# Performance work log

Measured on AMD Instinct MI355X. Metric: run time of the kernel, lower is better.

## Reference

```python
import jax, jax.numpy as jnp
import numpy as np

Q_DIM = 512
K_DIM = 512
HID = 512


def setup_inputs() -> dict:
    key = jax.random.key(0)
    k1, k2, k3, k4, k5, k6 = jax.random.split(key, 6)
    b, n_q, s = 4, 64, 1024
    queries = jax.random.normal(k1, (b, n_q, Q_DIM), dtype=jnp.float32)
    keys = jax.random.normal(k2, (b, s, K_DIM), dtype=jnp.float32)
    values = jax.random.normal(k3, (b, s, 512), dtype=jnp.float32)
    lim1 = 1.0 / np.sqrt(Q_DIM + K_DIM)
    W1 = jax.random.uniform(k4, (HID, Q_DIM + K_DIM), minval=-lim1, maxval=lim1, dtype=jnp.float32)
    b1 = jax.random.uniform(k5, (HID,), minval=-lim1, maxval=lim1, dtype=jnp.float32)
    lim2 = 1.0 / np.sqrt(HID)
    w2 = jax.random.uniform(k6, (HID,), minval=-lim2, maxval=lim2, dtype=jnp.float32)
    return {"queries": queries, "keys": keys, "values": values,
            "W1": W1, "b1": b1, "w2": w2}


def reference(queries, keys, values, W1, b1, w2):
    # linear1 on concat([q, k]) == W1q @ q + W1k @ k (split the weight),
    # avoiding materializing the concatenated [b, n_q, s, q_v+k_v] tensor.
    W1q = W1[:, :Q_DIM]  # [hid, q_dim]
    W1k = W1[:, Q_DIM:]  # [hid, k_dim]
    q_proj = jnp.einsum('bqd,hd->bqh', queries, W1q)          # [b, n_q, hid]
    k_proj = jnp.einsum('bsd,hd->bsh', keys, W1k) + b1        # [b, s, hid]
    hidden = jnp.tanh(q_proj[:, :, None, :] + k_proj[:, None, :, :])  # [b, n_q, s, hid]
    scores = jnp.einsum('bqsh,h->bqs', hidden, w2)            # [b, n_q, s]
    attn = jax.nn.softmax(scores, axis=2)                     # softmax over key axis
    final = jnp.einsum('bqs,bsv->bqv', attn, values)          # [b, n_q, v_dim]
    return final
```

## Files before the change

### kernel.cpp

```cpp
#include <hip/hip_runtime.h>


static constexpr int SLEN = 1024;
static constexpr int DIM  = 512;
static constexpr float TANH_SCALE = 2.885390081777927f;

typedef __attribute__((ext_vector_type(8))) short bf16x8;
typedef __attribute__((ext_vector_type(4))) float f32x4;

__device__ __forceinline__ float fast_exp2(float x) { return __builtin_amdgcn_exp2f(x); }
__device__ __forceinline__ float fast_rcp(float x)  { return __builtin_amdgcn_rcpf(x); }

__device__ __forceinline__ unsigned int f2bf(float f) {
    unsigned int u = __float_as_uint(f);
    u += 0x7FFF + ((u >> 16) & 1);
    return u >> 16;
}

__device__ __forceinline__ void async_copy16(const void* g, void* l) {
    __builtin_amdgcn_global_load_lds(
        (const __attribute__((address_space(1))) unsigned int*)g,
        (__attribute__((address_space(3))) unsigned int*)l, 16, 0, 0);
}

__global__ __launch_bounds__(256) void convert_bf16(
    const float* __restrict__ q, const float* __restrict__ k,
    const float* __restrict__ w, unsigned short* __restrict__ qb,
    unsigned short* __restrict__ kb, unsigned short* __restrict__ wb)
{
    int id = blockIdx.x * 256 + threadIdx.x;
    const float* src; unsigned short* dst; int off;
    if (id < 32768)        { src = q; dst = qb; off = id; }
    else if (id < 557056)  { src = k; dst = kb; off = id - 32768; }
    else                   { src = w; dst = wb; off = id - 557056; }
    float4 v = ((const float4*)src)[off];
    ushort4 o;
    o.x = (unsigned short)f2bf(v.x); o.y = (unsigned short)f2bf(v.y);
    o.z = (unsigned short)f2bf(v.z); o.w = (unsigned short)f2bf(v.w);
    ((ushort4*)dst)[off] = o;
}

__global__ __launch_bounds__(256) void proj_mfma(
    const unsigned short* __restrict__ qb, const unsigned short* __restrict__ kb,
    const unsigned short* __restrict__ wb, const float* __restrict__ b1,
    float* __restrict__ qp, float* __restrict__ kp)
{
    __shared__ __align__(16) unsigned short As[64][64];
    __shared__ __align__(16) unsigned short Ws[64][64];

    const int bx = blockIdx.x;
    const unsigned short* A; float* C; const float* bias; int mb, nb, col_off;
    if (bx < 512) {
        A = kb; C = kp; bias = b1; col_off = 512;
        mb = (bx >> 3) * 64; nb = (bx & 7) * 64;
    } else {
        int b2 = bx - 512;
        A = qb; C = qp; bias = nullptr; col_off = 0;
        mb = (b2 >> 3) * 64; nb = (b2 & 7) * 64;
    }

    const int t = threadIdx.x;
    const int l = t & 63;
    const int wv = t >> 6;
    const int wm = (wv & 1) * 32;
    const int wn = (wv >> 1) * 32;
    const int lane16 = l & 15;
    const int quad   = l >> 4;
    const int r8   = l >> 3;
    const int schk = (l & 7) ^ r8;

    f32x4 acc[2][2] = {{{0.f,0.f,0.f,0.f},{0.f,0.f,0.f,0.f}},
                       {{0.f,0.f,0.f,0.f},{0.f,0.f,0.f,0.f}}};

    for (int kc = 0; kc < DIM; kc += 64) {
#pragma unroll
        for (int i = 0; i < 2; ++i) {
            int rbase = wv * 16 + i * 8;
            async_copy16(A + (size_t)(mb + rbase + r8) * DIM + kc + schk * 8, &As[rbase][0]);
            async_copy16(wb + (size_t)(nb + rbase + r8) * 1024 + col_off + kc + schk * 8, &Ws[rbase][0]);
        }
        __syncthreads();

#pragma unroll
        for (int ks = 0; ks < 2; ++ks) {
            int cc = ks * 4 + quad;
            int sw = (cc ^ (lane16 & 7)) << 3;
            bf16x8 a0  = *(const bf16x8*)&As[wm + lane16][sw];
            bf16x8 a1  = *(const bf16x8*)&As[wm + 16 + lane16][sw];
            bf16x8 b0  = *(const bf16x8*)&Ws[wn + lane16][sw];
            bf16x8 b1v = *(const bf16x8*)&Ws[wn + 16 + lane16][sw];
            acc[0][0] = __builtin_amdgcn_mfma_f32_16x16x32_bf16(a0, b0,  acc[0][0], 0, 0, 0);
            acc[0][1] = __builtin_amdgcn_mfma_f32_16x16x32_bf16(a0, b1v, acc[0][1], 0, 0, 0);
            acc[1][0] = __builtin_amdgcn_mfma_f32_16x16x32_bf16(a1, b0,  acc[1][0], 0, 0, 0);
            acc[1][1] = __builtin_amdgcn_mfma_f32_16x16x32_bf16(a1, b1v, acc[1][1], 0, 0, 0);
        }
        __syncthreads();
    }

#pragma unroll
    for (int mi = 0; mi < 2; ++mi) {
#pragma unroll
        for (int ni = 0; ni < 2; ++ni) {
            int col = nb + wn + 16 * ni + lane16;
            float bv = bias ? bias[col] : 0.0f;
#pragma unroll
            for (int r = 0; r < 4; ++r) {
                int row = mb + wm + 16 * mi + quad * 4 + r;
                C[(size_t)row * DIM + col] = (acc[mi][ni][r] + bv) * TANH_SCALE;
            }
        }
    }
}

__global__ __launch_bounds__(256) void scores_kernel(
    const float* __restrict__ qp, const float* __restrict__ kp,
    const float* __restrict__ w2, float* __restrict__ sc)
{
    __shared__ __align__(16) float qs[16][68];
    __shared__ __align__(16) float ks[32][68];
    __shared__ __align__(16) float ws2[256];
    const int t     = threadIdx.x;
    const int sb    = blockIdx.x * 32;
    const int qt    = blockIdx.y & 3;
    const int half  = blockIdx.y >> 2;
    const int kbase = half * 256;
    const int qrow0 = blockIdx.z * 64 + qt * 16;
    const int krow0 = blockIdx.z * 1024 + sb;
    float* sch = sc + (size_t)half * 256 * SLEN;

    if (t < 64) *(float4*)&ws2[t << 2] = *(const float4*)(w2 + kbase + (t << 2));

    const int tq = t >> 4;
    const int ts = t & 15;
    float acc0 = 0.f, acc1 = 0.f;

    for (int kc = 0; kc < 256; kc += 64) {
        {
            int r = t >> 4, g = (t & 15) << 2;
            *(float4*)&qs[r][g] = *(const float4*)(qp + (size_t)(qrow0 + r) * DIM + kbase + kc + g);
        }
#pragma unroll
        for (int rr = 0; rr < 2; ++rr) {
            int idx = t + rr * 256;
            int r = idx >> 4, g = (idx & 15) << 2;
            *(float4*)&ks[r][g] = *(const float4*)(kp + (size_t)(krow0 + r) * DIM + kbase + kc + g);
        }
        __syncthreads();
#pragma unroll
        for (int k4 = 0; k4 < 16; ++k4) {
            float4 qv = *(const float4*)&qs[tq][k4 << 2];
            float4 k0 = *(const float4*)&ks[ts][k4 << 2];
            float4 k1 = *(const float4*)&ks[ts + 16][k4 << 2];
            float4 wv = *(const float4*)&ws2[kc + (k4 << 2)];
            acc0 = fmaf(wv.x, fast_rcp(1.0f + fast_exp2(qv.x + k0.x)), acc0);
            acc1 = fmaf(wv.x, fast_rcp(1.0f + fast_exp2(qv.x + k1.x)), acc1);
            acc0 = fmaf(wv.y, fast_rcp(1.0f + fast_exp2(qv.y + k0.y)), acc0);
            acc1 = fmaf(wv.y, fast_rcp(1.0f + fast_exp2(qv.y + k1.y)), acc1);
            acc0 = fmaf(wv.z, fast_rcp(1.0f + fast_exp2(qv.z + k0.z)), acc0);
            acc1 = fmaf(wv.z, fast_rcp(1.0f + fast_exp2(qv.z + k1.z)), acc1);
            acc0 = fmaf(wv.w, fast_rcp(1.0f + fast_exp2(qv.w + k0.w)), acc0);
            acc1 = fmaf(wv.w, fast_rcp(1.0f + fast_exp2(qv.w + k1.w)), acc1);
        }
        __syncthreads();
    }
    sch[(size_t)(qrow0 + tq) * SLEN + sb + ts]      = acc0;
    sch[(size_t)(qrow0 + tq) * SLEN + sb + ts + 16] = acc1;
}

__global__ __launch_bounds__(256) void softmax_kernel(
    const float* __restrict__ sc, float* __restrict__ attn)
{
    const int row = blockIdx.x;
    const int t   = threadIdx.x;
    __shared__ float redm[4];
    __shared__ float reds[4];
    float4 a = *(const float4*)(sc + (size_t)row * SLEN + (t << 2));
    float4 b = *(const float4*)(sc + (size_t)(256 + row) * SLEN + (t << 2));
    float4 v;
    v.x = a.x + b.x; v.y = a.y + b.y; v.z = a.z + b.z; v.w = a.w + b.w;
    float mn = fminf(fminf(v.x, v.y), fminf(v.z, v.w));
#pragma unroll
    for (int off = 32; off; off >>= 1) mn = fminf(mn, __shfl_xor(mn, off, 64));
    if ((t & 63) == 0) redm[t >> 6] = mn;
    __syncthreads();
    mn = fminf(fminf(redm[0], redm[1]), fminf(redm[2], redm[3]));
    float4 e;
    e.x = fast_exp2((mn - v.x) * TANH_SCALE);
    e.y = fast_exp2((mn - v.y) * TANH_SCALE);
    e.z = fast_exp2((mn - v.z) * TANH_SCALE);
    e.w = fast_exp2((mn - v.w) * TANH_SCALE);
    float s = e.x + e.y + e.z + e.w;
#pragma unroll
    for (int off = 32; off; off >>= 1) s += __shfl_xor(s, off, 64);
    if ((t & 63) == 0) reds[t >> 6] = s;
    __syncthreads();
    s = reds[0] + reds[1] + reds[2] + reds[3];
    float r = fast_rcp(s);
    e.x *= r; e.y *= r; e.z *= r; e.w *= r;
    *(float4*)(attn + (size_t)row * SLEN + (t << 2)) = e;
}

__global__ __launch_bounds__(256) void av_gemm(
    const float* __restrict__ attn, const float* __restrict__ values,
    float* __restrict__ pt)
{
    __shared__ __align__(16) float As[32][68];
    __shared__ __align__(16) float Bs[32][68];
    const int t  = threadIdx.x;
    const int nb = blockIdx.x * 64;
    const int kt = blockIdx.y;
    const int kb = kt * 128;
    const int b  = blockIdx.z;
    const int tx = t & 15, ty = t >> 4;
    float acc[4][4] = {};
    for (int kc = 0; kc < 128; kc += 32) {
        const int k0 = kb + kc;
#pragma unroll
        for (int r = 0; r < 2; ++r) {
            int idx = t + r * 256;
            int m   = idx >> 3;
            int k4  = (idx & 7) << 2;
            float4 av = *(const float4*)(attn + (size_t)(b * 64 + m) * SLEN + k0 + k4);
            As[k4 + 0][m] = av.x; As[k4 + 1][m] = av.y;
            As[k4 + 2][m] = av.z; As[k4 + 3][m] = av.w;
            int kk = idx >> 4;
            int g  = (idx & 15) << 2;
            *(float4*)&Bs[kk][g] =
                *(const float4*)(values + (size_t)(b * 1024 + k0 + kk) * DIM + nb + g);
        }
        __syncthreads();
#pragma unroll
        for (int k = 0; k < 32; ++k) {
            float4 a  = *(const float4*)&As[k][ty << 2];
            float4 bv = *(const float4*)&Bs[k][tx << 2];
            float am[4] = {a.x, a.y, a.z, a.w};
            float bn[4] = {bv.x, bv.y, bv.z, bv.w};
#pragma unroll
            for (int i = 0; i < 4; ++i)
#pragma unroll
                for (int j = 0; j < 4; ++j)
                    acc[i][j] = fmaf(am[i], bn[j], acc[i][j]);
        }
        __syncthreads();
    }
#pragma unroll
    for (int i = 0; i < 4; ++i) {
        int row = b * 64 + (ty << 2) + i;
        float4 o;
        o.x = acc[i][0]; o.y = acc[i][1]; o.z = acc[i][2]; o.w = acc[i][3];
        *(float4*)(pt + ((size_t)kt * 256 + row) * DIM + nb + (tx << 2)) = o;
    }
}

__global__ __launch_bounds__(256) void reduce_kernel(
    const float* __restrict__ pt, float* __restrict__ out)
{
    int idx = blockIdx.x * 256 + threadIdx.x;
    const float4* p = (const float4*)pt;
    float4 a = p[idx];
#pragma unroll
    for (int k = 1; k < 8; ++k) {
        float4 v = p[k * 32768 + idx];
        a.x += v.x; a.y += v.y; a.z += v.z; a.w += v.w;
    }
    ((float4*)out)[idx] = a;
}

extern "C" void kernel_launch(void* const* d_in, const int* in_sizes, int n_in,
                              void* d_out, int out_size, void* d_ws, size_t ws_size,
                              hipStream_t stream) {
    const float* queries = (const float*)d_in[0];
    const float* keys    = (const float*)d_in[1];
    const float* values  = (const float*)d_in[2];
    const float* W1      = (const float*)d_in[3];
    const float* b1      = (const float*)d_in[4];
    const float* w2      = (const float*)d_in[5];
    float* out = (float*)d_out;

    float* qp = (float*)d_ws;
    float* kp = qp + 256 * 512;
    float* sc = kp + 4096 * 512;
    float* at = sc + 2 * 256 * 1024;
    float* pt = at + 256 * 1024;
    unsigned short* qbf = (unsigned short*)(pt + 8 * 256 * 512);
    unsigned short* kbf = qbf + 256 * 512;
    unsigned short* wbf = kbf + 4096 * 512;
    (void)in_sizes; (void)n_in; (void)ws_size; (void)out_size;

    convert_bf16<<<dim3(2688), 256, 0, stream>>>(queries, keys, W1, qbf, kbf, wbf);
    proj_mfma<<<dim3(544), 256, 0, stream>>>(qbf, kbf, wbf, b1, qp, kp);
    scores_kernel<<<dim3(32, 8, 4), 256, 0, stream>>>(qp, kp, w2, sc);
    softmax_kernel<<<dim3(256), 256, 0, stream>>>(sc, at);
    av_gemm<<<dim3(8, 8, 4), 256, 0, stream>>>(at, values, pt);
    reduce_kernel<<<dim3(128), 256, 0, stream>>>(pt, out);
}
```

Before: 127.0 us.

## Fuse softmax into scores kernel and defer normalization to final reduce

The scores kernel now covers the full hidden dimension instead of splitting it in half. It applies the exponential directly, writing unnormalized weights, and accumulates per-row sums with atomics. Max subtraction is dropped, which is safe because the scores are bounded by the w2 magnitudes. The separate softmax kernel and its extra score buffer pass go away, and the row normalization moves into the final reduce. The costs are a memset, atomic contention on 256 sums, and half as many scores blocks.

```diff
diff --git a/kernel.cpp b/kernel.cpp
--- a/kernel.cpp
+++ b/kernel.cpp
@@ -114,36 +114,33 @@
 
 __global__ __launch_bounds__(256) void scores_kernel(
     const float* __restrict__ qp, const float* __restrict__ kp,
-    const float* __restrict__ w2, float* __restrict__ sc)
+    const float* __restrict__ w2, float* __restrict__ sc,
+    float* __restrict__ sums)
 {
     __shared__ __align__(16) float qs[16][68];
     __shared__ __align__(16) float ks[32][68];
-    __shared__ __align__(16) float ws2[256];
+    __shared__ __align__(16) float ws2[512];
     const int t     = threadIdx.x;
     const int sb    = blockIdx.x * 32;
-    const int qt    = blockIdx.y & 3;
-    const int half  = blockIdx.y >> 2;
-    const int kbase = half * 256;
-    const int qrow0 = blockIdx.z * 64 + qt * 16;
+    const int qrow0 = blockIdx.z * 64 + blockIdx.y * 16;
     const int krow0 = blockIdx.z * 1024 + sb;
-    float* sch = sc + (size_t)half * 256 * SLEN;
-
-    if (t < 64) *(float4*)&ws2[t << 2] = *(const float4*)(w2 + kbase + (t << 2));
+
+    if (t < 128) *(float4*)&ws2[t << 2] = *(const float4*)(w2 + (t << 2));
 
     const int tq = t >> 4;
     const int ts = t & 15;
     float acc0 = 0.f, acc1 = 0.f;
 
-    for (int kc = 0; kc < 256; kc += 64) {
+    for (int kc = 0; kc < DIM; kc += 64) {
         {
             int r = t >> 4, g = (t & 15) << 2;
-            *(float4*)&qs[r][g] = *(const float4*)(qp + (size_t)(qrow0 + r) * DIM + kbase + kc + g);
+            *(float4*)&qs[r][g] = *(const float4*)(qp + (size_t)(qrow0 + r) * DIM + kc + g);
         }
 #pragma unroll
         for (int rr = 0; rr < 2; ++rr) {
             int idx = t + rr * 256;
             int r = idx >> 4, g = (idx & 15) << 2;
-            *(float4*)&ks[r][g] = *(const float4*)(kp + (size_t)(krow0 + r) * DIM + kbase + kc + g);
+            *(float4*)&ks[r][g] = *(const float4*)(kp + (size_t)(krow0 + r) * DIM + kc + g);
         }
         __syncthreads();
 #pragma unroll
@@ -163,45 +160,19 @@
         }
         __syncthreads();
     }
-    sch[(size_t)(qrow0 + tq) * SLEN + sb + ts]      = acc0;
-    sch[(size_t)(qrow0 + tq) * SLEN + sb + ts + 16] = acc1;
-}
-
-__global__ __launch_bounds__(256) void softmax_kernel(
-    const float* __restrict__ sc, float* __restrict__ attn)
-{
-    const int row = blockIdx.x;
-    const int t   = threadIdx.x;
-    __shared__ float redm[4];
-    __shared__ float reds[4];
-    float4 a = *(const float4*)(sc + (size_t)row * SLEN + (t << 2));
-    float4 b = *(const float4*)(sc + (size_t)(256 + row) * SLEN + (t << 2));
-    float4 v;
-    v.x = a.x + b.x; v.y = a.y + b.y; v.z = a.z + b.z; v.w = a.w + b.w;
-    float mn = fminf(fminf(v.x, v.y), fminf(v.z, v.w));
-#pragma unroll
-    for (int off = 32; off; off >>= 1) mn = fminf(mn, __shfl_xor(mn, off, 64));
-    if ((t & 63) == 0) redm[t >> 6] = mn;
-    __syncthreads();
-    mn = fminf(fminf(redm[0], redm[1]), fminf(redm[2], redm[3]));
-    float4 e;
-    e.x = fast_exp2((mn - v.x) * TANH_SCALE);
-    e.y = fast_exp2((mn - v.y) * TANH_SCALE);
-    e.z = fast_exp2((mn - v.z) * TANH_SCALE);
-    e.w = fast_exp2((mn - v.w) * TANH_SCALE);
-    float s = e.x + e.y + e.z + e.w;
-#pragma unroll
-    for (int off = 32; off; off >>= 1) s += __shfl_xor(s, off, 64);
-    if ((t & 63) == 0) reds[t >> 6] = s;
-    __syncthreads();
-    s = reds[0] + reds[1] + reds[2] + reds[3];
-    float r = fast_rcp(s);
-    e.x *= r; e.y *= r; e.z *= r; e.w *= r;
-    *(float4*)(attn + (size_t)row * SLEN + (t << 2)) = e;
+    float e0 = fast_exp2(-TANH_SCALE * acc0);
+    float e1 = fast_exp2(-TANH_SCALE * acc1);
+    sc[(size_t)(qrow0 + tq) * SLEN + sb + ts]      = e0;
+    sc[(size_t)(qrow0 + tq) * SLEN + sb + ts + 16] = e1;
+
+    float rsum = e0 + e1;
+#pragma unroll
+    for (int m = 1; m < 16; m <<= 1) rsum += __shfl_xor(rsum, m, 64);
+    if (ts == 0) atomicAdd(&sums[qrow0 + tq], rsum);
 }
 
 __global__ __launch_bounds__(256) void av_gemm(
-    const float* __restrict__ attn, const float* __restrict__ values,
+    const float* __restrict__ e, const float* __restrict__ values,
     float* __restrict__ pt)
 {
     __shared__ __align__(16) float As[32][68];
@@ -220,7 +191,7 @@
             int idx = t + r * 256;
             int m   = idx >> 3;
             int k4  = (idx & 7) << 2;
-            float4 av = *(const float4*)(attn + (size_t)(b * 64 + m) * SLEN + k0 + k4);
+            float4 av = *(const float4*)(e + (size_t)(b * 64 + m) * SLEN + k0 + k4);
             As[k4 + 0][m] = av.x; As[k4 + 1][m] = av.y;
             As[k4 + 2][m] = av.z; As[k4 + 3][m] = av.w;
             int kk = idx >> 4;
@@ -253,7 +224,8 @@
 }
 
 __global__ __launch_bounds__(256) void reduce_kernel(
-    const float* __restrict__ pt, float* __restrict__ out)
+    const float* __restrict__ pt, const float* __restrict__ sums,
+    float* __restrict__ out)
 {
     int idx = blockIdx.x * 256 + threadIdx.x;
     const float4* p = (const float4*)pt;
@@ -263,6 +235,8 @@
         float4 v = p[k * 32768 + idx];
         a.x += v.x; a.y += v.y; a.z += v.z; a.w += v.w;
     }
+    float r = fast_rcp(sums[idx >> 7]);
+    a.x *= r; a.y *= r; a.z *= r; a.w *= r;
     ((float4*)out)[idx] = a;
 }
 
@@ -277,20 +251,20 @@
     const float* w2      = (const float*)d_in[5];
     float* out = (float*)d_out;
 
-    float* qp = (float*)d_ws;
-    float* kp = qp + 256 * 512;
-    float* sc = kp + 4096 * 512;
-    float* at = sc + 2 * 256 * 1024;
-    float* pt = at + 256 * 1024;
-    unsigned short* qbf = (unsigned short*)(pt + 8 * 256 * 512);
+    float* qp   = (float*)d_ws;
+    float* kp   = qp + 256 * 512;
+    float* sc   = kp + 4096 * 512;
+    float* pt   = sc + 256 * 1024;
+    float* sums = pt + 8 * 256 * 512;
+    unsigned short* qbf = (unsigned short*)(sums + 256);
     unsigned short* kbf = qbf + 256 * 512;
     unsigned short* wbf = kbf + 4096 * 512;
     (void)in_sizes; (void)n_in; (void)ws_size; (void)out_size;
 
+    hipMemsetAsync(sums, 0, 256 * sizeof(float), stream);
     convert_bf16<<<dim3(2688), 256, 0, stream>>>(queries, keys, W1, qbf, kbf, wbf);
     proj_mfma<<<dim3(544), 256, 0, stream>>>(qbf, kbf, wbf, b1, qp, kp);
-    scores_kernel<<<dim3(32, 8, 4), 256, 0, stream>>>(qp, kp, w2, sc);
-    softmax_kernel<<<dim3(256), 256, 0, stream>>>(sc, at);
-    av_gemm<<<dim3(8, 8, 4), 256, 0, stream>>>(at, values, pt);
-    reduce_kernel<<<dim3(128), 256, 0, stream>>>(pt, out);
-}
+    scores_kernel<<<dim3(32, 4, 4), 256, 0, stream>>>(qp, kp, w2, sc, sums);
+    av_gemm<<<dim3(8, 8, 4), 256, 0, stream>>>(sc, values, pt);
+    reduce_kernel<<<dim3(128), 256, 0, stream>>>(pt, sums, out);
+}
```

New measurement: 132.2 us. 4.1% more time.
